# Kernel tuning notes

Measured on AMD Instinct MI355X. Metric: run time of the kernel, lower is better.

Reference implementation:

```python
import jax, jax.numpy as jnp
import numpy as np

B, S, D = 16, 16, 4096
H, KV, HD = 32, 8, 128
MAX_B, MAX_S = 16, 4096
START = 4080


def setup_inputs() -> dict:
    key = jax.random.key(0)
    ks = jax.random.split(key, 10)
    sc = 0.02
    # RoPE angles for positions [START, START+S)
    inv_freq = 1.0 / (10000.0 ** (np.arange(0, HD, 2, dtype=np.float32) / HD))  # [HD/2]
    pos = np.arange(START, START + S, dtype=np.float32)
    ang = np.outer(pos, inv_freq)  # [S, HD/2]
    return {
        'x': jax.random.normal(ks[0], (B, S, D), jnp.float32),
        'k': jax.random.normal(ks[1], (B, S, D), jnp.float32),
        'v': jax.random.normal(ks[2], (B, S, D), jnp.float32),
        'wq': jax.random.normal(ks[3], (D, H * HD), jnp.float32) * sc,
        'wk': jax.random.normal(ks[4], (D, KV * HD), jnp.float32) * sc,
        'wv': jax.random.normal(ks[5], (D, KV * HD), jnp.float32) * sc,
        'wo': jax.random.normal(ks[6], (H * HD, D), jnp.float32) * sc,
        'cache_k': jax.random.normal(ks[7], (MAX_B, MAX_S, KV, HD), jnp.float32),
        'cache_v': jax.random.normal(ks[8], (MAX_B, MAX_S, KV, HD), jnp.float32),
        'freqs_cos': jnp.asarray(np.cos(ang)),
        'freqs_sin': jnp.asarray(np.sin(ang)),
        'start_pos': START,
    }


def _rope(t, cos, sin):
    # t: [B,S,nh,HD]; interleaved complex pairs (even=real, odd=imag)
    t2 = t.reshape(*t.shape[:-1], HD // 2, 2)
    x0, x1 = t2[..., 0], t2[..., 1]
    c = cos[None, :, None, :]
    s = sin[None, :, None, :]
    r0 = x0 * c - x1 * s
    r1 = x0 * s + x1 * c
    return jnp.stack([r0, r1], axis=-1).reshape(t.shape)


def reference(x, k, v, wq, wk, wv, wo, cache_k, cache_v, freqs_cos, freqs_sin, start_pos):
    rep = H // KV
    xq = (x @ wq).reshape(B, S, H, HD)
    xk = (k @ wk).reshape(B, S, KV, HD)
    xv = (v @ wv).reshape(B, S, KV, HD)
    xq = _rope(xq, freqs_cos, freqs_sin)
    xk = _rope(xk, freqs_cos, freqs_sin)
    # KV-cache append (start_pos is a static Python int)
    cache_k = jax.lax.dynamic_update_slice(cache_k, xk, (0, start_pos, 0, 0))
    cache_v = jax.lax.dynamic_update_slice(cache_v, xv, (0, start_pos, 0, 0))
    T = start_pos + S
    keys = cache_k[:B, :T]    # [B,T,KV,HD]
    values = cache_v[:B, :T]  # [B,T,KV,HD]
    # GQA without materializing repeat_kv: q head h = g*rep + r
    q = xq.reshape(B, S, KV, rep, HD)
    scores = jnp.einsum('bsgrd,btgd->bgrst', q, keys) / jnp.sqrt(jnp.float32(HD))
    attn = jax.nn.softmax(scores.astype(jnp.float32), axis=-1).astype(q.dtype)
    out = jnp.einsum('bgrst,btgd->bsgrd', attn, values).reshape(B, S, H * HD)
    return out @ wo
```

## Files before the change

### kernel.cpp

```cpp
#include <hip/hip_runtime.h>

typedef __attribute__((ext_vector_type(8))) short bf8_t;
typedef __attribute__((ext_vector_type(4))) short s4_t;
typedef __attribute__((ext_vector_type(4))) float f4_t;
typedef __attribute__((ext_vector_type(4))) unsigned u4_t;

#define DEV static __device__ __forceinline__

DEV short f2bf(float f) {
  union { float f; unsigned u; } x; x.f = f;
  unsigned r = x.u + 0x7FFFu + ((x.u >> 16) & 1u);
  return (short)(r >> 16);
}
DEV float bf2f(short h) {
  union { unsigned u; float f; } x; x.u = ((unsigned)(unsigned short)h) << 16;
  return x.f;
}
DEV unsigned pk2(float a, float b) {
  return (unsigned)(unsigned short)f2bf(a) |
         ((unsigned)(unsigned short)f2bf(b) << 16);
}
DEV f4_t mfma16(bf8_t a, bf8_t b, f4_t c) {
  return __builtin_amdgcn_mfma_f32_16x16x32_bf16(a, b, c, 0, 0, 0);
}
DEV f4_t zf4() { f4_t v = {0.f, 0.f, 0.f, 0.f}; return v; }

__global__ __launch_bounds__(256)
void prep_inputs(const float* __restrict__ x, const float* __restrict__ k,
                 const float* __restrict__ v, short* __restrict__ xb,
                 short* __restrict__ kb, short* __restrict__ vb)
{
  int gid = blockIdx.x * 256 + threadIdx.x;
  size_t base = (size_t)gid * 8;
  const float* src; short* dst; size_t off;
  if (base < 1048576)       { src = x; dst = xb; off = base; }
  else if (base < 2097152)  { src = k; dst = kb; off = base - 1048576; }
  else                      { src = v; dst = vb; off = base - 2097152; }
  f4_t f0 = *(const f4_t*)(src + off);
  f4_t f1 = *(const f4_t*)(src + off + 4);
  bf8_t hv;
#pragma unroll
  for (int j = 0; j < 4; j++) { hv[j] = f2bf(f0[j]); hv[4 + j] = f2bf(f1[j]); }
  *(bf8_t*)(dst + off) = hv;
}

__global__ __launch_bounds__(256, 4)
void qkv_kernel(const short* __restrict__ xb, const short* __restrict__ kb,
                const short* __restrict__ vb, const float* __restrict__ wq,
                const float* __restrict__ wk, const float* __restrict__ wv,
                float* __restrict__ part)
{
  __shared__ short Bs[2][64][40];

  int bid = blockIdx.x;
  int sw = (bid & 7) * 192 + (bid >> 3);
  int ks = sw / 384;
  int r  = sw % 384;

  int lin, N, cbase;
  const short* A; const float* W;
  if (r < 256)      { lin = r;       A = xb; W = wq; N = 4096; cbase = 0; }
  else if (r < 320) { lin = r - 256; A = kb; W = wk; N = 1024; cbase = 4096; }
  else              { lin = r - 320; A = vb; W = wv; N = 1024; cbase = 5120; }
  int m0 = (lin & 3) * 64;
  int n0 = (lin >> 2) * 64;
  int k0 = ks * 1024;

  int tid = threadIdx.x, w = tid >> 6, l = tid & 63;
  f4_t acc[4];
#pragma unroll
  for (int i = 0; i < 4; i++) acc[i] = zf4();

  int bn = tid & 63;
  int bch = (tid >> 6) ^ ((tid >> 3) & 3);
  int bk = bch * 8;
  const float* wptr = W + n0 + bn;

  const short* afrag = A + (m0 + w * 16 + (l & 15)) * 4096 + k0 + (l >> 4) * 8;

  bf8_t areg = *(const bf8_t*)afrag;
  float brA[8], brB[8];
#pragma unroll
  for (int j = 0; j < 8; j++) brA[j] = wptr[(size_t)(k0 + bk + j) * N];
#pragma unroll
  for (int j = 0; j < 8; j++) brB[j] = wptr[(size_t)(k0 + 32 + bk + j) * N];

  auto body = [&](int it, float (&br)[8], int buf) {
    {
      bf8_t hv;
#pragma unroll
      for (int j = 0; j < 8; j++) hv[j] = f2bf(br[j]);
      *(bf8_t*)&Bs[buf][bn][bk] = hv;
    }
    bf8_t ac = areg;
    if (it + 1 < 32) areg = *(const bf8_t*)(afrag + (it + 1) * 32);
    if (it + 2 < 32) {
#pragma unroll
      for (int j = 0; j < 8; j++)
        br[j] = wptr[(size_t)(k0 + (it + 2) * 32 + bk + j) * N];
    }
    __syncthreads();
    __builtin_amdgcn_s_setprio(1);
#pragma unroll
    for (int nt = 0; nt < 4; ++nt) {
      bf8_t bh = *(const bf8_t*)&Bs[buf][nt * 16 + (l & 15)][(l >> 4) * 8];
      acc[nt] = mfma16(ac, bh, acc[nt]);
    }
    __builtin_amdgcn_s_setprio(0);
  };

  for (int p = 0; p < 16; ++p) {
    body(2 * p,     brA, 0);
    body(2 * p + 1, brB, 1);
  }

  float* po = part + ((size_t)ks * 256 + m0) * 6144 + cbase + n0;
  int cl = l & 15, gq = l >> 4;
#pragma unroll
  for (int nt = 0; nt < 4; ++nt)
#pragma unroll
    for (int i = 0; i < 4; i++)
      po[(w * 16 + gq * 4 + i) * 6144 + nt * 16 + cl] = acc[nt][i];
}

__global__ __launch_bounds__(256)
void reduce_rope(const float* __restrict__ part,
                 const float* __restrict__ fcos, const float* __restrict__ fsin,
                 short* __restrict__ qh,
                 float* __restrict__ kf, float* __restrict__ vf)
{
  int gid = blockIdx.x * 256 + threadIdx.x;
  int row = gid / 768;
  int c8  = (gid - row * 768) * 8;
  const float* p = part + (size_t)row * 6144 + c8;
  float v[8];
#pragma unroll
  for (int j = 0; j < 8; j++) v[j] = p[j];
#pragma unroll
  for (int ksp = 1; ksp < 4; ksp++) {
    const float* q = p + (size_t)ksp * 256 * 6144;
#pragma unroll
    for (int j = 0; j < 8; j++) v[j] += q[j];
  }
  int s = row & 15, bb = row >> 4;
  if (c8 < 4096) {
    int h = c8 >> 7, d = c8 & 127;
    f4_t c  = *(const f4_t*)(fcos + s * 64 + (d >> 1));
    f4_t sn = *(const f4_t*)(fsin + s * 64 + (d >> 1));
    bf8_t hv;
#pragma unroll
    for (int pr = 0; pr < 4; pr++) {
      float x0 = v[2 * pr], x1 = v[2 * pr + 1];
      float r0 = (x0 * c[pr] - x1 * sn[pr]) * 0.08838834764831845f;
      float r1 = (x0 * sn[pr] + x1 * c[pr]) * 0.08838834764831845f;
      hv[2 * pr]     = f2bf(r0);
      hv[2 * pr + 1] = f2bf(r1);
    }
    int idx = ((bb * 8 + (h >> 2)) * 64 + (h & 3) * 16 + s) * 128 + d;
    *(bf8_t*)(qh + idx) = hv;
  } else if (c8 < 5120) {
    int cc = c8 - 4096; int h = cc >> 7, d = cc & 127;
    f4_t c  = *(const f4_t*)(fcos + s * 64 + (d >> 1));
    f4_t sn = *(const f4_t*)(fsin + s * 64 + (d >> 1));
    f4_t o0, o1;
#pragma unroll
    for (int pr = 0; pr < 2; pr++) {
      float x0 = v[2 * pr], x1 = v[2 * pr + 1];
      o0[2 * pr]     = x0 * c[pr] - x1 * sn[pr];
      o0[2 * pr + 1] = x0 * sn[pr] + x1 * c[pr];
    }
#pragma unroll
    for (int pr = 2; pr < 4; pr++) {
      float x0 = v[2 * pr], x1 = v[2 * pr + 1];
      o1[2 * (pr - 2)]     = x0 * c[pr] - x1 * sn[pr];
      o1[2 * (pr - 2) + 1] = x0 * sn[pr] + x1 * c[pr];
    }
    size_t idx = (((size_t)bb * 16 + s) * 8 + h) * 128 + d;
    *(f4_t*)(kf + idx) = o0;
    *(f4_t*)(kf + idx + 4) = o1;
  } else {
    int cc = c8 - 5120; int h = cc >> 7, d = cc & 127;
    size_t idx = (((size_t)bb * 16 + s) * 8 + h) * 128 + d;
    f4_t o0, o1;
#pragma unroll
    for (int j = 0; j < 4; j++) { o0[j] = v[j]; o1[j] = v[4 + j]; }
    *(f4_t*)(vf + idx) = o0;
    *(f4_t*)(vf + idx + 4) = o1;
  }
}

__global__ __launch_bounds__(256, 3)
void attn_kernel(const float* __restrict__ ck, const float* __restrict__ cv,
                 const short* __restrict__ qhp,
                 const float* __restrict__ kfp, const float* __restrict__ vfp,
                 const int* __restrict__ startp,
                 float* __restrict__ Op, float* __restrict__ mp,
                 float* __restrict__ lp)
{
  __shared__ short Kh[32][136];
  __shared__ short Vt[128][40];
  __shared__ short Ps[4][16][40];

  int bid = blockIdx.x;
  int bg = bid >> 3, sp = bid & 7;
  int b = bg >> 3, g = bg & 7;
  int tid = threadIdx.x, w = tid >> 6, l = tid & 63;
  int start = *startp;

  bf8_t qfh[4];
  {
    int qoff = (bg * 64 + w * 16 + (l & 15)) * 128 + (l >> 4) * 8;
#pragma unroll
    for (int kt = 0; kt < 4; ++kt)
      qfh[kt] = *(const bf8_t*)(qhp + qoff + kt * 32);
  }
  f4_t of[8];
#pragma unroll
  for (int i = 0; i < 8; i++) of[i] = zf4();
  float mrun[4], lrun[4];
#pragma unroll
  for (int i = 0; i < 4; i++) { mrun[i] = -1e30f; lrun[i] = 0.f; }

  int st_t = tid >> 3;
  int d0   = (tid & 7) * 16;
  int rr   = (tid >> 3) & 7;
  int oo   = tid >> 6;
  int vunit = ((oo ^ (tid & 7)) & 3) * 8;

  f4_t kr[4], vr[4];

  auto ISSUE = [&](int tile) {
    int t = sp * 512 + tile * 32 + st_t;
    size_t o_st = (((size_t)b * 4096 + t) * 8 + g) * 128;
    size_t o_fr = (((size_t)b * 16 + (size_t)(t - start)) * 8 + g) * 128;
    const float* kp_ = (t < start) ? (ck + o_st) : (kfp + o_fr);
    const float* vp_ = (t < start) ? (cv + o_st) : (vfp + o_fr);
#pragma unroll
    for (int j = 0; j < 4; j++) kr[j] = *(const f4_t*)(kp_ + d0 + 4 * j);
#pragma unroll
    for (int j = 0; j < 4; j++) vr[j] = *(const f4_t*)(vp_ + d0 + 4 * j);
  };

  auto WRITE = [&]() {
    unsigned kp[8];
#pragma unroll
    for (int p = 0; p < 8; p++)
      kp[p] = pk2(kr[p >> 1][(p & 1) * 2], kr[p >> 1][(p & 1) * 2 + 1]);
    u4_t kw0 = {kp[0], kp[1], kp[2], kp[3]};
    u4_t kw1 = {kp[4], kp[5], kp[6], kp[7]};
    *(u4_t*)&Kh[st_t][d0] = kw0;
    *(u4_t*)&Kh[st_t][d0 + 8] = kw1;

    unsigned vp[8];
#pragma unroll
    for (int p = 0; p < 8; p++)
      vp[p] = pk2(vr[p >> 1][(p & 1) * 2], vr[p >> 1][(p & 1) * 2 + 1]);
#pragma unroll
    for (int kk = 1; kk < 8; kk <<= 1) {
      unsigned nv[8];
#pragma unroll
      for (int i = 0; i < 8; i++) {
        unsigned ex = __shfl_xor(vp[i ^ kk], kk * 8);
        bool swp = (((i & kk) != 0) != ((rr & kk) != 0));
        nv[i] = swp ? ex : vp[i];
      }
#pragma unroll
      for (int i = 0; i < 8; i++) vp[i] = nv[i];
    }
    u4_t ra, rb;
#pragma unroll
    for (int i = 0; i < 4; i++) {
      ra[i] = (vp[2 * i] & 0xffffu) | (vp[2 * i + 1] << 16);
      rb[i] = (vp[2 * i] >> 16) | (vp[2 * i + 1] & 0xffff0000u);
    }
    *(u4_t*)&Vt[d0 + 2 * rr][vunit] = ra;
    *(u4_t*)&Vt[d0 + 2 * rr + 1][vunit] = rb;
  };

  ISSUE(0);
  WRITE();
  __syncthreads();
  ISSUE(1);

  for (int tile = 0; tile < 16; ++tile) {
    f4_t sf[2];
#pragma unroll
    for (int i = 0; i < 2; i++) sf[i] = zf4();
    __builtin_amdgcn_s_setprio(1);
#pragma unroll
    for (int tt = 0; tt < 2; ++tt)
#pragma unroll
      for (int kt = 0; kt < 4; ++kt) {
        bf8_t kb = *(const bf8_t*)&Kh[tt * 16 + (l & 15)][kt * 32 + (l >> 4) * 8];
        sf[tt] = mfma16(qfh[kt], kb, sf[tt]);
      }
    __builtin_amdgcn_s_setprio(0);

    float mt[4];
#pragma unroll
    for (int i = 0; i < 4; i++) mt[i] = fmaxf(sf[0][i], sf[1][i]);
#pragma unroll
    for (int st = 1; st < 16; st <<= 1)
#pragma unroll
      for (int i = 0; i < 4; i++) mt[i] = fmaxf(mt[i], __shfl_xor(mt[i], st));
    float sc[4];
#pragma unroll
    for (int i = 0; i < 4; i++) {
      float mn = fmaxf(mrun[i], mt[i]);
      sc[i] = __expf(mrun[i] - mn);
      mrun[i] = mn;
    }
    float rs[4] = {0.f, 0.f, 0.f, 0.f};
#pragma unroll
    for (int tt = 0; tt < 2; ++tt)
#pragma unroll
      for (int i = 0; i < 4; i++) {
        float pexp = __expf(sf[tt][i] - mrun[i]);
        rs[i] += pexp;
        Ps[w][(l >> 4) * 4 + i][tt * 16 + (l & 15)] = f2bf(pexp);
      }
#pragma unroll
    for (int st = 1; st < 16; st <<= 1)
#pragma unroll
      for (int i = 0; i < 4; i++) rs[i] += __shfl_xor(rs[i], st);
#pragma unroll
    for (int i = 0; i < 4; i++) lrun[i] = lrun[i] * sc[i] + rs[i];
#pragma unroll
    for (int dt = 0; dt < 8; ++dt)
#pragma unroll
      for (int i = 0; i < 4; i++) of[dt][i] *= sc[i];

    __builtin_amdgcn_s_setprio(1);
    {
      bf8_t pa = *(const bf8_t*)&Ps[w][l & 15][(l >> 4) * 8];
#pragma unroll
      for (int dt = 0; dt < 8; ++dt) {
        bf8_t vfr = *(const bf8_t*)&Vt[dt * 16 + (l & 15)][(((l >> 4) ^ dt) & 3) * 8];
        of[dt] = mfma16(pa, vfr, of[dt]);
      }
    }
    __builtin_amdgcn_s_setprio(0);

    if (tile < 15) {
      __syncthreads();
      WRITE();
      __syncthreads();
      if (tile < 14) ISSUE(tile + 2);
    }
  }

  size_t obase = ((size_t)(bg * 8 + sp) * 64 + w * 16) * 128;
#pragma unroll
  for (int dt = 0; dt < 8; ++dt)
#pragma unroll
    for (int i = 0; i < 4; i++)
      Op[obase + ((l >> 4) * 4 + i) * 128 + dt * 16 + (l & 15)] = of[dt][i];
  if ((l & 15) == 0) {
    int rbase = (bg * 8 + sp) * 64 + w * 16 + (l >> 4) * 4;
#pragma unroll
    for (int i = 0; i < 4; i++) { mp[rbase + i] = mrun[i]; lp[rbase + i] = lrun[i]; }
  }
}

__global__ __launch_bounds__(256)
void merge_kernel(const float* __restrict__ Op, const float* __restrict__ mp,
                  const float* __restrict__ lp, short* __restrict__ attnb)
{
  int bid = blockIdx.x;
  int bg = bid >> 2, q4 = bid & 3;
  int tid = threadIdx.x;
  int row = q4 * 16 + (tid >> 4);
  int dc = (tid & 15) * 8;
  int b = bg >> 3, g = bg & 7;
  int r = row >> 4, s = row & 15;
  float mm[8], ww[8];
  float M = -1e30f;
#pragma unroll
  for (int spp = 0; spp < 8; ++spp) {
    mm[spp] = mp[(bg * 8 + spp) * 64 + row];
    M = fmaxf(M, mm[spp]);
  }
  float denom = 0.f;
#pragma unroll
  for (int spp = 0; spp < 8; ++spp) {
    ww[spp] = __expf(mm[spp] - M);
    denom += lp[(bg * 8 + spp) * 64 + row] * ww[spp];
  }
  float inv = 1.0f / denom;
  f4_t a0 = zf4(), a1 = zf4();
#pragma unroll
  for (int spp = 0; spp < 8; ++spp) {
    const float* o = Op + ((size_t)(bg * 8 + spp) * 64 + row) * 128 + dc;
    f4_t x0 = *(const f4_t*)o;
    f4_t x1 = *(const f4_t*)(o + 4);
#pragma unroll
    for (int i = 0; i < 4; i++) { a0[i] += ww[spp] * x0[i]; a1[i] += ww[spp] * x1[i]; }
  }
  int ob = (b * 16 + s) * 4096 + (g * 4 + r) * 128 + dc;
  bf8_t o8;
#pragma unroll
  for (int i = 0; i < 4; i++) {
    o8[i]     = f2bf(a0[i] * inv);
    o8[4 + i] = f2bf(a1[i] * inv);
  }
  *(bf8_t*)(attnb + ob) = o8;
}

__global__ __launch_bounds__(256, 3)
void wo_kernel(const short* __restrict__ attnb, const float* __restrict__ wo,
               float* __restrict__ out)
{
  __shared__ short Bs[2][64][40];

  int bid = blockIdx.x;
  int lin = (bid & 7) * 64 + (bid >> 3);
  int m0 = (lin & 7) * 32, n0 = (lin >> 3) * 64;

  int tid = threadIdx.x, w = tid >> 6, l = tid & 63;
  f4_t acc[2];
#pragma unroll
  for (int i = 0; i < 2; i++) acc[i] = zf4();

  int bn = tid & 63;
  int bch = (tid >> 6) ^ ((tid >> 3) & 3);
  int bk = bch * 8;
  const float* wptr = wo + n0 + bn;
  int n32 = (w >> 1) * 32;
  const short* afrag = attnb + (m0 + (w & 1) * 16 + (l & 15)) * 4096 + (l >> 4) * 8;

  bf8_t areg = *(const bf8_t*)afrag;
  float brA[8], brB[8];
#pragma unroll
  for (int j = 0; j < 8; j++) brA[j] = wptr[(size_t)(bk + j) * 4096];
#pragma unroll
  for (int j = 0; j < 8; j++) brB[j] = wptr[(size_t)(32 + bk + j) * 4096];

  auto body = [&](int it, float (&br)[8], int buf) {
    {
      bf8_t hv;
#pragma unroll
      for (int j = 0; j < 8; j++) hv[j] = f2bf(br[j]);
      *(bf8_t*)&Bs[buf][bn][bk] = hv;
    }
    bf8_t ac = areg;
    if (it + 1 < 128) areg = *(const bf8_t*)(afrag + (it + 1) * 32);
    if (it + 2 < 128) {
#pragma unroll
      for (int j = 0; j < 8; j++)
        br[j] = wptr[(size_t)((it + 2) * 32 + bk + j) * 4096];
    }
    __syncthreads();
    __builtin_amdgcn_s_setprio(1);
#pragma unroll
    for (int nt = 0; nt < 2; ++nt) {
      bf8_t bb_ = *(const bf8_t*)&Bs[buf][n32 + nt * 16 + (l & 15)][(l >> 4) * 8];
      acc[nt] = mfma16(ac, bb_, acc[nt]);
    }
    __builtin_amdgcn_s_setprio(0);
  };

  for (int p = 0; p < 64; ++p) {
    body(2 * p,     brA, 0);
    body(2 * p + 1, brB, 1);
  }

  int cl = l & 15, gq = l >> 4;
#pragma unroll
  for (int nt = 0; nt < 2; ++nt)
#pragma unroll
    for (int i = 0; i < 4; i++)
      out[(m0 + (w & 1) * 16 + gq * 4 + i) * 4096 + n0 + n32 + nt * 16 + cl] =
          acc[nt][i];
}

extern "C" void kernel_launch(void* const* d_in, const int* in_sizes, int n_in,
                              void* d_out, int out_size, void* d_ws, size_t ws_size,
                              hipStream_t stream)
{
  const float* x  = (const float*)d_in[0];
  const float* k  = (const float*)d_in[1];
  const float* v  = (const float*)d_in[2];
  const float* wq = (const float*)d_in[3];
  const float* wk = (const float*)d_in[4];
  const float* wv = (const float*)d_in[5];
  const float* wo = (const float*)d_in[6];
  const float* ck = (const float*)d_in[7];
  const float* cv = (const float*)d_in[8];
  const float* fc = (const float*)d_in[9];
  const float* fs = (const float*)d_in[10];
  const int*   spv = (const int*)d_in[11];
  float* out = (float*)d_out;

  char* p = (char*)d_ws;
  float* S = (float*)p; p += (size_t)1024 * 64 * 128 * 4;
  float* qpart = S;
  float* Op    = S;
  short* xb = (short*)p; p += (size_t)256 * 4096 * 2;
  short* kb = (short*)p; p += (size_t)256 * 4096 * 2;
  short* vb = (short*)p; p += (size_t)256 * 4096 * 2;
  short* qh = (short*)p; p += (size_t)128 * 64 * 128 * 2;
  float* kf = (float*)p; p += (size_t)256 * 8 * 128 * 4;
  float* vf = (float*)p; p += (size_t)256 * 8 * 128 * 4;
  short* attnb = (short*)p; p += (size_t)256 * 4096 * 2;
  float* mp = (float*)p; p += (size_t)1024 * 64 * 4;
  float* lp = (float*)p; p += (size_t)1024 * 64 * 4;

  hipLaunchKernelGGL(prep_inputs, dim3(1536), dim3(256), 0, stream,
                     x, k, v, xb, kb, vb);
  hipLaunchKernelGGL(qkv_kernel, dim3(1536), dim3(256), 0, stream,
                     xb, kb, vb, wq, wk, wv, qpart);
  hipLaunchKernelGGL(reduce_rope, dim3(768), dim3(256), 0, stream,
                     qpart, fc, fs, qh, kf, vf);
  hipLaunchKernelGGL(attn_kernel, dim3(1024), dim3(256), 0, stream,
                     ck, cv, qh, kf, vf, spv, Op, mp, lp);
  hipLaunchKernelGGL(merge_kernel, dim3(512), dim3(256), 0, stream,
                     Op, mp, lp, attnb);
  hipLaunchKernelGGL(wo_kernel, dim3(512), dim3(256), 0, stream,
                     attnb, wo, out);
}
```

Baseline: 288.2 us.

## Use cheaper bf16 packing, lazy softmax rescale, and raise attention occupancy

```diff
diff --git a/kernel.cpp b/kernel.cpp
--- a/kernel.cpp
+++ b/kernel.cpp
@@ -1,24 +1,18 @@
 #include <hip/hip_runtime.h>
 
 typedef __attribute__((ext_vector_type(8))) short bf8_t;
-typedef __attribute__((ext_vector_type(4))) short s4_t;
 typedef __attribute__((ext_vector_type(4))) float f4_t;
 typedef __attribute__((ext_vector_type(4))) unsigned u4_t;
 
 #define DEV static __device__ __forceinline__
 
-DEV short f2bf(float f) {
-  union { float f; unsigned u; } x; x.f = f;
-  unsigned r = x.u + 0x7FFFu + ((x.u >> 16) & 1u);
-  return (short)(r >> 16);
-}
-DEV float bf2f(short h) {
-  union { unsigned u; float f; } x; x.u = ((unsigned)(unsigned short)h) << 16;
-  return x.f;
-}
 DEV unsigned pk2(float a, float b) {
-  return (unsigned)(unsigned short)f2bf(a) |
-         ((unsigned)(unsigned short)f2bf(b) << 16);
+  unsigned ua = __float_as_uint(a) + 0x8000u;
+  unsigned ub = __float_as_uint(b) + 0x8000u;
+  return __builtin_amdgcn_perm(ub, ua, 0x07060302u);
+}
+DEV short bf1(float a) {
+  return (short)((__float_as_uint(a) + 0x8000u) >> 16);
 }
 DEV f4_t mfma16(bf8_t a, bf8_t b, f4_t c) {
   return __builtin_amdgcn_mfma_f32_16x16x32_bf16(a, b, c, 0, 0, 0);
@@ -38,10 +32,10 @@
   else                      { src = v; dst = vb; off = base - 2097152; }
   f4_t f0 = *(const f4_t*)(src + off);
   f4_t f1 = *(const f4_t*)(src + off + 4);
-  bf8_t hv;
-#pragma unroll
-  for (int j = 0; j < 4; j++) { hv[j] = f2bf(f0[j]); hv[4 + j] = f2bf(f1[j]); }
-  *(bf8_t*)(dst + off) = hv;
+  u4_t hv;
+  hv[0] = pk2(f0[0], f0[1]); hv[1] = pk2(f0[2], f0[3]);
+  hv[2] = pk2(f1[0], f1[1]); hv[3] = pk2(f1[2], f1[3]);
+  *(u4_t*)(dst + off) = hv;
 }
 
 __global__ __launch_bounds__(256, 4)
@@ -87,10 +81,10 @@
 
   auto body = [&](int it, float (&br)[8], int buf) {
     {
-      bf8_t hv;
-#pragma unroll
-      for (int j = 0; j < 8; j++) hv[j] = f2bf(br[j]);
-      *(bf8_t*)&Bs[buf][bn][bk] = hv;
+      u4_t hv;
+      hv[0] = pk2(br[0], br[1]); hv[1] = pk2(br[2], br[3]);
+      hv[2] = pk2(br[4], br[5]); hv[3] = pk2(br[6], br[7]);
+      *(u4_t*)&Bs[buf][bn][bk] = hv;
     }
     bf8_t ac = areg;
     if (it + 1 < 32) areg = *(const bf8_t*)(afrag + (it + 1) * 32);
@@ -147,17 +141,16 @@
     int h = c8 >> 7, d = c8 & 127;
     f4_t c  = *(const f4_t*)(fcos + s * 64 + (d >> 1));
     f4_t sn = *(const f4_t*)(fsin + s * 64 + (d >> 1));
-    bf8_t hv;
+    u4_t hv;
 #pragma unroll
     for (int pr = 0; pr < 4; pr++) {
       float x0 = v[2 * pr], x1 = v[2 * pr + 1];
       float r0 = (x0 * c[pr] - x1 * sn[pr]) * 0.08838834764831845f;
       float r1 = (x0 * sn[pr] + x1 * c[pr]) * 0.08838834764831845f;
-      hv[2 * pr]     = f2bf(r0);
-      hv[2 * pr + 1] = f2bf(r1);
+      hv[pr] = pk2(r0, r1);
     }
     int idx = ((bb * 8 + (h >> 2)) * 64 + (h & 3) * 16 + s) * 128 + d;
-    *(bf8_t*)(qh + idx) = hv;
+    *(u4_t*)(qh + idx) = hv;
   } else if (c8 < 5120) {
     int cc = c8 - 4096; int h = cc >> 7, d = cc & 127;
     f4_t c  = *(const f4_t*)(fcos + s * 64 + (d >> 1));
@@ -189,7 +182,7 @@
   }
 }
 
-__global__ __launch_bounds__(256, 3)
+__global__ __launch_bounds__(256, 4)
 void attn_kernel(const float* __restrict__ ck, const float* __restrict__ cv,
                  const short* __restrict__ qhp,
                  const float* __restrict__ kfp, const float* __restrict__ vfp,
@@ -242,12 +235,11 @@
   };
 
   auto WRITE = [&]() {
-    unsigned kp[8];
-#pragma unroll
-    for (int p = 0; p < 8; p++)
-      kp[p] = pk2(kr[p >> 1][(p & 1) * 2], kr[p >> 1][(p & 1) * 2 + 1]);
-    u4_t kw0 = {kp[0], kp[1], kp[2], kp[3]};
-    u4_t kw1 = {kp[4], kp[5], kp[6], kp[7]};
+    u4_t kw0, kw1;
+    kw0[0] = pk2(kr[0][0], kr[0][1]); kw0[1] = pk2(kr[0][2], kr[0][3]);
+    kw0[2] = pk2(kr[1][0], kr[1][1]); kw0[3] = pk2(kr[1][2], kr[1][3]);
+    kw1[0] = pk2(kr[2][0], kr[2][1]); kw1[1] = pk2(kr[2][2], kr[2][3]);
+    kw1[2] = pk2(kr[3][0], kr[3][1]); kw1[3] = pk2(kr[3][2], kr[3][3]);
     *(u4_t*)&Kh[st_t][d0] = kw0;
     *(u4_t*)&Kh[st_t][d0 + 8] = kw1;
 
@@ -303,13 +295,22 @@
     for (int st = 1; st < 16; st <<= 1)
 #pragma unroll
       for (int i = 0; i < 4; i++) mt[i] = fmaxf(mt[i], __shfl_xor(mt[i], st));
-    float sc[4];
-#pragma unroll
-    for (int i = 0; i < 4; i++) {
-      float mn = fmaxf(mrun[i], mt[i]);
-      sc[i] = __expf(mrun[i] - mn);
-      mrun[i] = mn;
-    }
+
+    bool need = false;
+#pragma unroll
+    for (int i = 0; i < 4; i++) need = need || (mt[i] > mrun[i] + 8.0f);
+    if (__any(need)) {
+#pragma unroll
+      for (int i = 0; i < 4; i++) {
+        float mn = fmaxf(mrun[i], mt[i]);
+        float sc = __expf(mrun[i] - mn);
+        mrun[i] = mn;
+        lrun[i] *= sc;
+#pragma unroll
+        for (int dt = 0; dt < 8; ++dt) of[dt][i] *= sc;
+      }
+    }
+
     float rs[4] = {0.f, 0.f, 0.f, 0.f};
 #pragma unroll
     for (int tt = 0; tt < 2; ++tt)
@@ -317,18 +318,14 @@
       for (int i = 0; i < 4; i++) {
         float pexp = __expf(sf[tt][i] - mrun[i]);
         rs[i] += pexp;
-        Ps[w][(l >> 4) * 4 + i][tt * 16 + (l & 15)] = f2bf(pexp);
+        Ps[w][(l >> 4) * 4 + i][tt * 16 + (l & 15)] = bf1(pexp);
       }
 #pragma unroll
     for (int st = 1; st < 16; st <<= 1)
 #pragma unroll
       for (int i = 0; i < 4; i++) rs[i] += __shfl_xor(rs[i], st);
 #pragma unroll
-    for (int i = 0; i < 4; i++) lrun[i] = lrun[i] * sc[i] + rs[i];
-#pragma unroll
-    for (int dt = 0; dt < 8; ++dt)
-#pragma unroll
-      for (int i = 0; i < 4; i++) of[dt][i] *= sc[i];
+    for (int i = 0; i < 4; i++) lrun[i] += rs[i];
 
     __builtin_amdgcn_s_setprio(1);
     {
@@ -397,13 +394,12 @@
     for (int i = 0; i < 4; i++) { a0[i] += ww[spp] * x0[i]; a1[i] += ww[spp] * x1[i]; }
   }
   int ob = (b * 16 + s) * 4096 + (g * 4 + r) * 128 + dc;
-  bf8_t o8;
-#pragma unroll
-  for (int i = 0; i < 4; i++) {
-    o8[i]     = f2bf(a0[i] * inv);
-    o8[4 + i] = f2bf(a1[i] * inv);
-  }
-  *(bf8_t*)(attnb + ob) = o8;
+  u4_t o8;
+  o8[0] = pk2(a0[0] * inv, a0[1] * inv);
+  o8[1] = pk2(a0[2] * inv, a0[3] * inv);
+  o8[2] = pk2(a1[0] * inv, a1[1] * inv);
+  o8[3] = pk2(a1[2] * inv, a1[3] * inv);
+  *(u4_t*)(attnb + ob) = o8;
 }
 
 __global__ __launch_bounds__(256, 3)
@@ -437,10 +433,10 @@
 
   auto body = [&](int it, float (&br)[8], int buf) {
     {
-      bf8_t hv;
-#pragma unroll
-      for (int j = 0; j < 8; j++) hv[j] = f2bf(br[j]);
-      *(bf8_t*)&Bs[buf][bn][bk] = hv;
+      u4_t hv;
+      hv[0] = pk2(br[0], br[1]); hv[1] = pk2(br[2], br[3]);
+      hv[2] = pk2(br[4], br[5]); hv[3] = pk2(br[6], br[7]);
+      *(u4_t*)&Bs[buf][bn][bk] = hv;
     }
     bf8_t ac = areg;
     if (it + 1 < 128) areg = *(const bf8_t*)(afrag + (it + 1) * 32);
```

New measurement: 291.2 us. About the same (+1.0%).
